# Kernel optimization log

Measured on AMD Instinct MI355X. Metric: run time of the kernel, lower is better.

## Reference

```python
import jax, jax.numpy as jnp
import numpy as np

REG_MAX = 16
BOX_W = 7.5
OBJ_W = 1.0
TOPK = 10
EPS = 1e-7


def dfl_decode(x, reg_max):
    # x: [B, 4*reg_max, N] -> expected value of per-side distribution -> [B, N, 4] (xyxy)
    B, C, N = x.shape
    x = x.reshape(B, 4, reg_max, N)
    p = jax.nn.softmax(x, axis=2)
    proj = jnp.arange(reg_max, dtype=x.dtype)
    return jnp.einsum('bkrn,r->bnk', p, proj)


def bbox_ciou(b1, b2):
    # b1: [B,N,1,4], b2: [B,1,M,4], xyxy -> [B,N,M]
    x11, y11, x12, y12 = b1[..., 0], b1[..., 1], b1[..., 2], b1[..., 3]
    x21, y21, x22, y22 = b2[..., 0], b2[..., 1], b2[..., 2], b2[..., 3]
    w1, h1 = x12 - x11, y12 - y11
    w2, h2 = x22 - x21, y22 - y21
    iw = jnp.clip(jnp.minimum(x12, x22) - jnp.maximum(x11, x21), 0.0)
    ih = jnp.clip(jnp.minimum(y12, y22) - jnp.maximum(y11, y21), 0.0)
    inter = iw * ih
    union = w1 * h1 + w2 * h2 - inter + EPS
    iou = inter / union
    cw = jnp.maximum(x12, x22) - jnp.minimum(x11, x21)
    ch = jnp.maximum(y12, y22) - jnp.minimum(y11, y21)
    c2 = cw * cw + ch * ch + EPS
    rho2 = ((x21 + x22 - x11 - x12) ** 2 + (y21 + y22 - y11 - y12) ** 2) * 0.25
    v = (4.0 / (np.pi ** 2)) * (jnp.arctan(w2 / (h2 + EPS)) - jnp.arctan(w1 / (h1 + EPS))) ** 2
    alpha = jax.lax.stop_gradient(v / (v - iou + 1.0 + EPS))
    return iou - rho2 / c2 - alpha * v


def setup_inputs() -> dict:
    key = jax.random.key(0)
    k1, k2, k3, k4 = jax.random.split(key, 4)
    B, N, M = 8, 34000, 64
    boxes = jax.random.normal(k1, (B, 4 * REG_MAX, N), dtype=jnp.float32)
    scores = jax.random.normal(k2, (B, N), dtype=jnp.float32)
    # GT boxes: valid xyxy in roughly the same [0, reg_max) range as decoded preds
    xy = jax.random.uniform(k3, (B, M, 2), dtype=jnp.float32) * 11.0
    wh = jax.random.uniform(k4, (B, M, 2), dtype=jnp.float32) * 4.0 + 0.5
    targets = jnp.concatenate([xy, xy + wh], axis=-1)
    return {'boxes': boxes, 'scores': scores, 'targets': targets}


def reference(boxes, scores, targets):
    B, N = scores.shape
    M = targets.shape[1]
    pb = dfl_decode(boxes, REG_MAX)                     # [B,N,4]
    ciou = bbox_ciou(pb[:, :, None, :], targets[:, None, :, :])  # [B,N,M]
    k = min(TOPK, N)
    topv, topi = jax.lax.top_k(jnp.swapaxes(ciou, 1, 2), k)      # [B,M,k] over anchors
    valid = topv > 0.0
    vals = jnp.where(valid, topv, 0.0)

    def per_batch(idx, val, vld):
        flat_i = idx.reshape(-1)
        iou_t = jnp.zeros((N,), val.dtype).at[flat_i].max(val.reshape(-1))
        pos = jnp.zeros((N,), bool).at[flat_i].max(vld.reshape(-1))
        return iou_t, pos

    iou_target, pos = jax.vmap(per_batch)(topi, vals, valid)     # [B,N]
    posf = pos.astype(iou_target.dtype)
    npos = posf.sum(axis=1)
    box_per = jnp.where(npos > 0,
                        ((1.0 - iou_target) * posf).sum(axis=1) / jnp.maximum(npos, 1.0),
                        0.0)
    box_loss = box_per.sum()
    # BCEWithLogits (mean over anchors), summed over batch
    bce = jnp.maximum(scores, 0.0) - scores * iou_target + jnp.log1p(jnp.exp(-jnp.abs(scores)))
    obj_loss = bce.mean(axis=1).sum()
    total = (BOX_W * box_loss + OBJ_W * obj_loss) / B
    return total, box_loss, obj_loss
```

## Files before the change

### kernel.cpp

```cpp
#include <hip/hip_runtime.h>
#include <math.h>

#define BQ 8
#define MQ 64
#define REGMAX 16
#define KTOP 10
#define EPSQ 1e-7f
#define APB 256
#define MBUF 1344

__device__ __forceinline__ float frcp(float x) { return __builtin_amdgcn_rcpf(x); }

#define DECL_LOAD16(P, G)                                                      \
  float G##0 = (P)[0], G##1 = (P)[Ns], G##2 = (P)[2 * Ns], G##3 = (P)[3 * Ns], \
        G##4 = (P)[4 * Ns], G##5 = (P)[5 * Ns], G##6 = (P)[6 * Ns],            \
        G##7 = (P)[7 * Ns], G##8 = (P)[8 * Ns], G##9 = (P)[9 * Ns],            \
        G##10 = (P)[10 * Ns], G##11 = (P)[11 * Ns], G##12 = (P)[12 * Ns],      \
        G##13 = (P)[13 * Ns], G##14 = (P)[14 * Ns], G##15 = (P)[15 * Ns];

#define EV16(G, OUT)                                                           \
  {                                                                            \
    float mx = fmaxf(fmaxf(fmaxf(fmaxf(G##0, G##1), fmaxf(G##2, G##3)),        \
                           fmaxf(fmaxf(G##4, G##5), fmaxf(G##6, G##7))),       \
                     fmaxf(fmaxf(fmaxf(G##8, G##9), fmaxf(G##10, G##11)),      \
                           fmaxf(fmaxf(G##12, G##13), fmaxf(G##14, G##15))));  \
    float s = 0.f, ws = 0.f, e;                                                \
    e = __expf(G##0 - mx); s += e;                                             \
    e = __expf(G##1 - mx); s += e; ws += 1.f * e;                              \
    e = __expf(G##2 - mx); s += e; ws += 2.f * e;                              \
    e = __expf(G##3 - mx); s += e; ws += 3.f * e;                              \
    e = __expf(G##4 - mx); s += e; ws += 4.f * e;                              \
    e = __expf(G##5 - mx); s += e; ws += 5.f * e;                              \
    e = __expf(G##6 - mx); s += e; ws += 6.f * e;                              \
    e = __expf(G##7 - mx); s += e; ws += 7.f * e;                              \
    e = __expf(G##8 - mx); s += e; ws += 8.f * e;                              \
    e = __expf(G##9 - mx); s += e; ws += 9.f * e;                              \
    e = __expf(G##10 - mx); s += e; ws += 10.f * e;                            \
    e = __expf(G##11 - mx); s += e; ws += 11.f * e;                            \
    e = __expf(G##12 - mx); s += e; ws += 12.f * e;                            \
    e = __expf(G##13 - mx); s += e; ws += 13.f * e;                            \
    e = __expf(G##14 - mx); s += e; ws += 14.f * e;                            \
    e = __expf(G##15 - mx); s += e; ws += 15.f * e;                            \
    OUT = ws * frcp(s);                                                        \
  }

__global__ __launch_bounds__(256) void decode_topk_kernel(
    const float* __restrict__ boxes, const float* __restrict__ scores,
    const float* __restrict__ targets, unsigned int* __restrict__ iou_bits,
    uint2* __restrict__ cand, float* __restrict__ bcePartial,
    unsigned int* __restrict__ ctr, int N, int bpb) {
  const int tid = threadIdx.x;
  const int b = blockIdx.x / bpb;
  const int blk = blockIdx.x - b * bpb;
  const int a0 = blk * APB;
  const int w = tid >> 6;
  const int l = tid & 63;

  __shared__ float4 s_sv[APB];
  __shared__ float s_at[APB];
  __shared__ int s_ix[APB];
  __shared__ float s_hv[4 * MQ * KTOP];
  __shared__ int s_hi[4 * MQ * KTOP];
  __shared__ uint2 s_mg[MQ * KTOP];
  __shared__ int s_cnt;
  __shared__ float s_bce;
  if (tid == 0) { s_cnt = 0; s_bce = 0.f; }
  if (blockIdx.x == 0 && tid == 0) *ctr = 0u;
  __syncthreads();

  const int n = a0 + tid;
  float bce0 = 0.f;
  bool pred = false;
  float e0 = 0.f, e1 = 0.f, e2 = 0.f, e3 = 0.f, at = 0.f;
  if (n < N) {
    const size_t i = (size_t)b * N + n;
    iou_bits[i] = 0u;
    const size_t Ns = (size_t)N;
    const float* base = boxes + (size_t)(b * 64) * Ns + n;
    const float* p0 = base;
    const float* p1 = base + 16 * Ns;
    const float* p2 = base + 32 * Ns;
    const float* p3 = base + 48 * Ns;
    DECL_LOAD16(p0, a)
    DECL_LOAD16(p1, bv)
    DECL_LOAD16(p2, c)
    DECL_LOAD16(p3, d)
    float sc = scores[i];
    bce0 = fmaxf(sc, 0.f) + log1pf(__expf(-fabsf(sc)));
    EV16(a, e0)
    EV16(bv, e1)
    EV16(c, e2)
    EV16(d, e3)
    float w1 = e2 - e0, h1 = e3 - e1;
    if (w1 > 0.f && h1 > 0.f) {
      pred = true;
      at = atanf(w1 * frcp(h1 + EPSQ));
    }
  }
  {
    unsigned long long mask = __ballot(pred);
    int cnt = __popcll(mask);
    int bslot = 0;
    if (l == 0 && cnt) bslot = atomicAdd(&s_cnt, cnt);
    bslot = __shfl(bslot, 0, 64);
    if (pred) {
      int pos = bslot + __popcll(mask & ((1ull << l) - 1ull));
      s_sv[pos] = make_float4(e0, e1, e2, e3);
      s_at[pos] = at;
      s_ix[pos] = n;
    }
  }
#pragma unroll
  for (int d = 1; d < 64; d <<= 1) bce0 += __shfl_xor(bce0, d, 64);
  if (l == 0) atomicAdd(&s_bce, bce0);
  __syncthreads();
  const int nsurv = s_cnt;
  if (tid == 0) bcePartial[blockIdx.x] = s_bce;

  const float4 t = ((const float4*)targets)[b * MQ + l];
  const float x21 = t.x, y21 = t.y, x22 = t.z, y22 = t.w;
  const float w2 = x22 - x21, h2 = y22 - y21;
  const float atan_t = atanf(w2 * frcp(h2 + EPSQ));
  const float area2 = w2 * h2, sumx2 = x21 + x22, sumy2 = y21 + y22;
  const float CPI = 4.0f / (float)(M_PI * M_PI);

  float hv0 = 0.f, hv1 = 0.f, hv2 = 0.f, hv3 = 0.f, hv4 = 0.f;
  float hv5 = 0.f, hv6 = 0.f, hv7 = 0.f, hv8 = 0.f, hv9 = 0.f;
  int hi0 = 0, hi1 = 0, hi2 = 0, hi3 = 0, hi4 = 0;
  int hi5 = 0, hi6 = 0, hi7 = 0, hi8 = 0, hi9 = 0;

  const int qlen = (nsurv + 3) >> 2;
  const int j0 = w * qlen;
  const int j1 = min(nsurv, j0 + qlen);
  for (int j = j0; j < j1; ++j) {
    float4 p = s_sv[j];
    float pa = s_at[j];
    int ixj = s_ix[j];
    float x11 = p.x, y11 = p.y, x12 = p.z, y12 = p.w;
    float w1 = x12 - x11, h1 = y12 - y11;
    float iw = fmaxf(fminf(x12, x22) - fmaxf(x11, x21), 0.f);
    float ih = fmaxf(fminf(y12, y22) - fmaxf(y11, y21), 0.f);
    float inter = iw * ih;
    float uni = w1 * h1 + area2 - inter + EPSQ;
    float iou = inter * frcp(uni);
    float cw = fmaxf(x12, x22) - fminf(x11, x21);
    float ch = fmaxf(y12, y22) - fminf(y11, y21);
    float c2 = cw * cw + ch * ch + EPSQ;
    float dx = sumx2 - x11 - x12;
    float dy = sumy2 - y11 - y12;
    float rho2 = (dx * dx + dy * dy) * 0.25f;
    float da = atan_t - pa;
    float v = CPI * da * da;
    float alpha = v * frcp(v - iou + 1.f + EPSQ);
    float ciou = iou - rho2 * frcp(c2) - alpha * v;
    if (ciou > hv9) {
      float cv = ciou;
      int ci = ixj;
#define INS(vk, ik)                         \
  {                                         \
    bool gt = cv > vk;                      \
    float tv_ = vk; int ti_ = ik;           \
    vk = gt ? cv : vk; ik = gt ? ci : ik;   \
    cv = gt ? tv_ : cv; ci = gt ? ti_ : ci; \
  }
      INS(hv0, hi0) INS(hv1, hi1) INS(hv2, hi2) INS(hv3, hi3) INS(hv4, hi4)
      INS(hv5, hi5) INS(hv6, hi6) INS(hv7, hi7) INS(hv8, hi8) INS(hv9, hi9)
#undef INS
    }
  }
  const int hb = (w * MQ + l) * KTOP;
  s_hv[hb + 0] = hv0; s_hi[hb + 0] = hi0;
  s_hv[hb + 1] = hv1; s_hi[hb + 1] = hi1;
  s_hv[hb + 2] = hv2; s_hi[hb + 2] = hi2;
  s_hv[hb + 3] = hv3; s_hi[hb + 3] = hi3;
  s_hv[hb + 4] = hv4; s_hi[hb + 4] = hi4;
  s_hv[hb + 5] = hv5; s_hi[hb + 5] = hi5;
  s_hv[hb + 6] = hv6; s_hi[hb + 6] = hi6;
  s_hv[hb + 7] = hv7; s_hi[hb + 7] = hi7;
  s_hv[hb + 8] = hv8; s_hi[hb + 8] = hi8;
  s_hv[hb + 9] = hv9; s_hi[hb + 9] = hi9;
  __syncthreads();

  if (w == 0) {
    const int m = l;
    int p0 = 0, p1 = 0, p2 = 0, p3 = 0;
    for (int r = 0; r < KTOP; ++r) {
      float c0 = s_hv[(0 * MQ + m) * KTOP + p0];
      float c1 = s_hv[(1 * MQ + m) * KTOP + p1];
      float c2m = s_hv[(2 * MQ + m) * KTOP + p2];
      float c3 = s_hv[(3 * MQ + m) * KTOP + p3];
      float best = c0; int bw = 0;
      if (c1 > best) { best = c1; bw = 1; }
      if (c2m > best) { best = c2m; bw = 2; }
      if (c3 > best) { best = c3; bw = 3; }
      int psel = (bw == 0) ? p0 : (bw == 1) ? p1 : (bw == 2) ? p2 : p3;
      int bidx = s_hi[(bw * MQ + m) * KTOP + psel];
      s_mg[m * KTOP + r] = make_uint2(__float_as_uint(best), (unsigned)bidx);
      if (bw == 0) p0 = min(p0 + 1, KTOP - 1);
      else if (bw == 1) p1 = min(p1 + 1, KTOP - 1);
      else if (bw == 2) p2 = min(p2 + 1, KTOP - 1);
      else p3 = min(p3 + 1, KTOP - 1);
    }
  }
  __syncthreads();
  uint2* obase = cand + (size_t)(b * bpb + blk) * (MQ * KTOP);
  for (int sl = tid; sl < MQ * KTOP; sl += 256) obase[sl] = s_mg[sl];
}

__device__ __forceinline__ void select_top10(
    float* s_bv, int* s_bi, float* s_winv, int* s_wini,
    int* s_cnt, int c, int tid) {
  if (tid < 64) {
    for (int r = 0; r < KTOP; ++r) {
      float bv = 0.f;
      int bs = 0xffff;
      for (int sl = tid; sl < c; sl += 64) {
        float v = s_bv[sl];
        if (v > bv) { bv = v; bs = sl; }
      }
      unsigned long long key =
          ((unsigned long long)__float_as_uint(bv) << 32) | (unsigned int)bs;
#pragma unroll
      for (int d = 1; d < 64; d <<= 1) {
        unsigned long long o = __shfl_xor(key, d, 64);
        if (o > key) key = o;
      }
      if (tid == 0) {
        float wv = __uint_as_float((unsigned int)(key >> 32));
        int ws = (int)(key & 0xffffu);
        s_winv[r] = wv;
        if (wv > 0.f && ws != 0xffff) {
          s_wini[r] = s_bi[ws];
          s_bv[ws] = 0.f;
        } else {
          s_wini[r] = 0;
        }
      }
    }
    if (tid < KTOP) { s_bv[tid] = s_winv[tid]; s_bi[tid] = s_wini[tid]; }
    if (tid == 0) *s_cnt = KTOP;
  }
}

__global__ __launch_bounds__(256) void merge_kernel(
    const uint2* __restrict__ cand, const float* __restrict__ scores,
    unsigned int* __restrict__ iou_bits, const float* __restrict__ bcePartial,
    float* __restrict__ mergePartial, unsigned int* __restrict__ ctr,
    float* __restrict__ out, int N, int bpb) {
  const int bm = blockIdx.x;
  const int b = bm >> 6;
  const int m = bm & 63;
  const int tid = threadIdx.x;
  const int l = tid & 63;
  const int NC = bpb * KTOP;

  __shared__ float s_bv[MBUF];
  __shared__ int s_bi[MBUF];
  __shared__ float s_winv[KTOP];
  __shared__ int s_wini[KTOP];
  __shared__ int s_cnt;
  __shared__ float s_d[3];
  __shared__ int s_last;
  __shared__ float s_acc[BQ * 3];
  if (tid == 0) s_cnt = 0;
  if (tid < 3) s_d[tid] = 0.f;
  if (tid < BQ * 3) s_acc[tid] = 0.f;
  __syncthreads();

  for (int k2 = tid; k2 < NC; k2 += 256) {
    int blkk = k2 / KTOP;
    int r = k2 - blkk * KTOP;
    uint2 e = cand[((size_t)(b * bpb + blkk) * MQ + m) * KTOP + r];
    float v = __uint_as_float(e.x);
    bool p = v > 0.f;
    unsigned long long mask = __ballot(p);
    int cnt = __popcll(mask);
    int bslot = 0;
    if (l == 0 && cnt) bslot = atomicAdd(&s_cnt, cnt);
    bslot = __shfl(bslot, 0, 64);
    if (p) {
      int pos = bslot + __popcll(mask & ((1ull << l) - 1ull));
      s_bv[pos] = v;
      s_bi[pos] = (int)e.y;
    }
  }
  __syncthreads();
  int c = s_cnt;
  __syncthreads();
  if (c > KTOP) {
    select_top10(s_bv, s_bi, s_winv, s_wini, &s_cnt, c, tid);
    __syncthreads();
    c = KTOP;
  }
  if (tid < KTOP && tid < c) {
    float v = s_bv[tid];
    if (v > 0.f) {
      int ix = s_bi[tid];
      unsigned int vb = __float_as_uint(v);
      unsigned int old = atomicMax(&iou_bits[(size_t)b * N + ix], vb);
      if (old < vb) {
        float vold = __uint_as_float(old);
        bool was = (old != 0u);
        atomicAdd(&s_d[0], was ? (vold - v) : (1.f - v));
        if (!was) atomicAdd(&s_d[1], 1.f);
        atomicAdd(&s_d[2], -scores[(size_t)b * N + ix] * (v - vold));
      }
    }
  }
  __syncthreads();
  if (tid == 0) {
    float4* mp = (float4*)(mergePartial + (size_t)bm * 4);
    *mp = make_float4(s_d[0], s_d[1], s_d[2], 0.f);
    __threadfence();
    unsigned int done = atomicAdd(ctr, 1u);
    s_last = (done == (unsigned)(gridDim.x - 1)) ? 1 : 0;
  }
  __syncthreads();
  if (s_last) {
    __threadfence();
    volatile const float* mp = mergePartial;
    for (int i = tid; i < BQ * MQ; i += 256) {
      int bb = i >> 6;
      float a0 = mp[i * 4 + 0];
      float a1 = mp[i * 4 + 1];
      float a2 = mp[i * 4 + 2];
      atomicAdd(&s_acc[bb * 3 + 0], a0);
      atomicAdd(&s_acc[bb * 3 + 1], a1);
      atomicAdd(&s_acc[bb * 3 + 2], a2);
    }
    volatile const float* bp = bcePartial;
    for (int i = tid; i < BQ * bpb; i += 256) {
      int bb = i / bpb;
      atomicAdd(&s_acc[bb * 3 + 2], bp[i]);
    }
    __syncthreads();
    if (tid == 0) {
      float box = 0.f, obj = 0.f;
      for (int bb = 0; bb < BQ; ++bb) {
        float np = s_acc[bb * 3 + 1];
        box += (np > 0.f) ? s_acc[bb * 3 + 0] / fmaxf(np, 1.f) : 0.f;
        obj += s_acc[bb * 3 + 2] / (float)N;
      }
      out[0] = (7.5f * box + obj) / (float)BQ;
      out[1] = box;
      out[2] = obj;
    }
  }
}

extern "C" void kernel_launch(void* const* d_in, const int* in_sizes, int n_in,
                              void* d_out, int out_size, void* d_ws, size_t ws_size,
                              hipStream_t stream) {
  const float* boxes = (const float*)d_in[0];
  const float* scores = (const float*)d_in[1];
  const float* targets = (const float*)d_in[2];
  float* out = (float*)d_out;
  const int N = in_sizes[1] / BQ;

  const int bpb = (N + APB - 1) / APB;
  const int nblk = BQ * bpb;

  char* ws = (char*)d_ws;
  size_t cand_bytes = (size_t)BQ * bpb * MQ * KTOP * sizeof(uint2);
  size_t iou_bytes = (size_t)BQ * N * sizeof(unsigned int);
  size_t bce_bytes = (((size_t)nblk * sizeof(float)) + 255) & ~(size_t)255;
  size_t mp_bytes = (size_t)BQ * MQ * 4 * sizeof(float);

  uint2* cand = (uint2*)ws;                    ws += cand_bytes;
  unsigned int* iou_bits = (unsigned int*)ws;  ws += iou_bytes;
  float* bcePartial = (float*)ws;              ws += bce_bytes;
  float* mergePartial = (float*)ws;            ws += mp_bytes;
  unsigned int* ctr = (unsigned int*)ws;

  decode_topk_kernel<<<nblk, 256, 0, stream>>>(boxes, scores, targets,
                                               iou_bits, cand, bcePartial, ctr, N, bpb);
  merge_kernel<<<BQ * MQ, 256, 0, stream>>>(cand, scores, iou_bits, bcePartial,
                                            mergePartial, ctr, out, N, bpb);
}
```

Baseline: 142.5 us.

## Stream DFL logits through LDS with double-buffered global_load_lds

Replaces the 64 direct per-thread global loads of DFL logits with per-wave asynchronous global-to-LDS dword loads, double-buffered in two 16-row groups so each side's softmax overlaps the loads for the next side. The top-k scratch arrays are aliased into the same 32KB union buffer to keep LDS use flat. This is meant to cut VGPR pressure and hide memory latency. In exchange it adds manual waitcnt and sched_barrier control. Out-of-range columns are clamped to N-1.

```diff
diff --git a/kernel.cpp b/kernel.cpp
--- a/kernel.cpp
+++ b/kernel.cpp
@@ -3,7 +3,6 @@
 
 #define BQ 8
 #define MQ 64
-#define REGMAX 16
 #define KTOP 10
 #define EPSQ 1e-7f
 #define APB 256
@@ -11,12 +10,36 @@
 
 __device__ __forceinline__ float frcp(float x) { return __builtin_amdgcn_rcpf(x); }
 
-#define DECL_LOAD16(P, G)                                                      \
-  float G##0 = (P)[0], G##1 = (P)[Ns], G##2 = (P)[2 * Ns], G##3 = (P)[3 * Ns], \
-        G##4 = (P)[4 * Ns], G##5 = (P)[5 * Ns], G##6 = (P)[6 * Ns],            \
-        G##7 = (P)[7 * Ns], G##8 = (P)[8 * Ns], G##9 = (P)[9 * Ns],            \
-        G##10 = (P)[10 * Ns], G##11 = (P)[11 * Ns], G##12 = (P)[12 * Ns],      \
-        G##13 = (P)[13 * Ns], G##14 = (P)[14 * Ns], G##15 = (P)[15 * Ns];
+__device__ __forceinline__ void load_lds_dword(const float* g, void* l) {
+  __builtin_amdgcn_global_load_lds(
+      (const __attribute__((address_space(1))) void*)g,
+      (__attribute__((address_space(3))) void*)l, 4, 0, 0);
+}
+
+#define WAITVM(N)                                           \
+  asm volatile("s_waitcnt vmcnt(" #N ")" ::: "memory");     \
+  __builtin_amdgcn_sched_barrier(0);
+
+#define WAITLGKM()                                          \
+  asm volatile("s_waitcnt lgkmcnt(0)" ::: "memory");        \
+  __builtin_amdgcn_sched_barrier(0);
+
+#define G16(R0, BUF)                                                     \
+  {                                                                      \
+    _Pragma("unroll") for (int r = 0; r < 16; ++r)                       \
+        load_lds_dword(gl + (size_t)((R0) + r) * Ns, (BUF) + r * 64);    \
+    __builtin_amdgcn_sched_barrier(0);                                   \
+  }
+
+#define DECL_B(BUF, G)                                                   \
+  float G##0 = (BUF)[0 * 64 + l], G##1 = (BUF)[1 * 64 + l],              \
+        G##2 = (BUF)[2 * 64 + l], G##3 = (BUF)[3 * 64 + l],              \
+        G##4 = (BUF)[4 * 64 + l], G##5 = (BUF)[5 * 64 + l],              \
+        G##6 = (BUF)[6 * 64 + l], G##7 = (BUF)[7 * 64 + l],              \
+        G##8 = (BUF)[8 * 64 + l], G##9 = (BUF)[9 * 64 + l],              \
+        G##10 = (BUF)[10 * 64 + l], G##11 = (BUF)[11 * 64 + l],          \
+        G##12 = (BUF)[12 * 64 + l], G##13 = (BUF)[13 * 64 + l],          \
+        G##14 = (BUF)[14 * 64 + l], G##15 = (BUF)[15 * 64 + l];
 
 #define EV16(G, OUT)                                                           \
   {                                                                            \
@@ -56,46 +79,56 @@
   const int w = tid >> 6;
   const int l = tid & 63;
 
+  __shared__ __align__(16) char u_raw[32768];
+  float* s_hv = (float*)u_raw;
+  int* s_hi = (int*)(u_raw + 10240);
+  uint2* s_mg = (uint2*)(u_raw + 20480);
   __shared__ float4 s_sv[APB];
   __shared__ float s_at[APB];
   __shared__ int s_ix[APB];
-  __shared__ float s_hv[4 * MQ * KTOP];
-  __shared__ int s_hi[4 * MQ * KTOP];
-  __shared__ uint2 s_mg[MQ * KTOP];
   __shared__ int s_cnt;
   __shared__ float s_bce;
   if (tid == 0) { s_cnt = 0; s_bce = 0.f; }
   if (blockIdx.x == 0 && tid == 0) *ctr = 0u;
   __syncthreads();
 
+  const size_t Ns = (size_t)N;
+  float* wbuf0 = (float*)(u_raw + w * 8192);
+  float* wbuf1 = wbuf0 + 1024;
+
   const int n = a0 + tid;
+  const int colc = min(a0 + w * 64 + l, N - 1);
+  const float* gl = boxes + (size_t)(b * 64) * Ns + colc;
+
+  float e0, e1, e2, e3;
+  G16(0, wbuf0)
+  G16(16, wbuf1)
+  WAITVM(16)
+  { DECL_B(wbuf0, A) EV16(A, e0) }
+  WAITLGKM()
+  G16(32, wbuf0)
+  WAITVM(16)
+  { DECL_B(wbuf1, Bv) EV16(Bv, e1) }
+  WAITLGKM()
+  G16(48, wbuf1)
+  WAITVM(16)
+  { DECL_B(wbuf0, Cv) EV16(Cv, e2) }
+  WAITVM(0)
+  { DECL_B(wbuf1, Dv) EV16(Dv, e3) }
+
   float bce0 = 0.f;
   bool pred = false;
-  float e0 = 0.f, e1 = 0.f, e2 = 0.f, e3 = 0.f, at = 0.f;
+  float at = 0.f;
   if (n < N) {
-    const size_t i = (size_t)b * N + n;
-    iou_bits[i] = 0u;
-    const size_t Ns = (size_t)N;
-    const float* base = boxes + (size_t)(b * 64) * Ns + n;
-    const float* p0 = base;
-    const float* p1 = base + 16 * Ns;
-    const float* p2 = base + 32 * Ns;
-    const float* p3 = base + 48 * Ns;
-    DECL_LOAD16(p0, a)
-    DECL_LOAD16(p1, bv)
-    DECL_LOAD16(p2, c)
-    DECL_LOAD16(p3, d)
-    float sc = scores[i];
-    bce0 = fmaxf(sc, 0.f) + log1pf(__expf(-fabsf(sc)));
-    EV16(a, e0)
-    EV16(bv, e1)
-    EV16(c, e2)
-    EV16(d, e3)
     float w1 = e2 - e0, h1 = e3 - e1;
     if (w1 > 0.f && h1 > 0.f) {
       pred = true;
       at = atanf(w1 * frcp(h1 + EPSQ));
     }
+    const size_t i = (size_t)b * N + n;
+    iou_bits[i] = 0u;
+    float sc = scores[i];
+    bce0 = fmaxf(sc, 0.f) + log1pf(__expf(-fabsf(sc)));
   }
   {
     unsigned long long mask = __ballot(pred);
```

Measured after the change: 144.6 us. About the same (+1.5%).
